# Performance work log

Measured on AMD Instinct MI355X. Metric: run time of the kernel, lower is better.

Reference implementation:

```python
import jax, jax.numpy as jnp
import numpy as np

BETA = 1.0
EPS_MU = 1e-6
EPS_LOG = 1e-8
D_DIM = 2048
M_EVENTS = 16384
T_HORIZON = 100


def setup_inputs() -> dict:
    key = jax.random.key(0)
    k1, k2 = jax.random.split(key)
    # sorted event times in [0, T_HORIZON)
    t_events = jnp.sort(jax.random.uniform(k1, (M_EVENTS,), jnp.float32) * T_HORIZON)
    marks = jax.random.randint(k2, (M_EVENTS,), 0, D_DIM)  # int marks in {0..D-1}
    # learned params, init exactly as in torch module
    log_mu = jnp.full((D_DIM,), -3.0, jnp.float32)
    log_alpha = jnp.full((D_DIM, D_DIM), -4.0, jnp.float32)
    return {
        "t_events": t_events,
        "marks": marks,
        "T_max": T_HORIZON,
        "log_mu": log_mu,
        "log_alpha": log_alpha,
    }


def _loglik(t_events, log_mu, log_alpha, marks, T_max, beta=BETA):
    mu = jax.nn.softplus(log_mu) + EPS_MU          # [D]
    alpha = jax.nn.softplus(log_alpha)             # [D, D]
    D = mu.shape[0]
    # dt[0] = 0 so the first step leaves S (= zeros) untouched, matching the
    # torch loop which skips decay at n == 0.
    dt = jnp.concatenate([jnp.zeros((1,), t_events.dtype), jnp.diff(t_events)])  # [M]

    def step(S, xs):
        dt_n, d = xs
        S = jnp.exp(-beta * dt_n) * S              # exponential decay of state [D]
        lam_d = mu[d] + alpha[d] @ S               # intensity at event's mark
        S = S.at[d].add(1.0)                       # self-excitation bump
        return S, jnp.log(lam_d + EPS_LOG)

    _, log_lams = jax.lax.scan(step, jnp.zeros((D,), mu.dtype), (dt, marks))

    # compensator integral term
    T = jnp.asarray(T_max, t_events.dtype)
    one_minus_exp = 1.0 - jnp.exp(-beta * (T - t_events))          # [M]
    contrib = jax.ops.segment_sum(one_minus_exp, marks, num_segments=D)  # [D]
    integral = mu * T + alpha @ (contrib / beta)                   # [D]
    return log_lams.sum() - integral.sum()


def reference(t_events, marks, T_max, log_mu, log_alpha):
    return _loglik(t_events, log_mu, log_alpha, marks, T_max)
```

## Files before the change

kernel.cpp:

```cpp
#include <hip/hip_runtime.h>
#include <math.h>

#define D_DIM 2048
#define M_EV  16384
#define LCH   32
#define CCH   (M_EV / LCH)
#define SEG   32
#define NSEG  (CCH / SEG)
#define BETA  1.0f

__device__ __forceinline__ float softplus_f(float x){
  float e = __expf(-fabsf(x));
  return fmaxf(x, 0.0f) + __logf(1.0f + e);
}

__device__ __forceinline__ unsigned short f2bf(float f){
  unsigned b = __float_as_uint(f);
  return (unsigned short)((b + 0x7FFFu + ((b >> 16) & 1u)) >> 16);
}
__device__ __forceinline__ float bf2f(unsigned short u){
  return __uint_as_float(((unsigned)u) << 16);
}

__device__ __forceinline__ float decode_T(const void* p){
  unsigned bits = *(const unsigned*)p;
  float fv = __uint_as_float(bits);
  return (fv >= 1e-3f && fv <= 1e7f) ? fv : (float)(int)bits;
}

__device__ __forceinline__ float wave_red(float v){
  #pragma unroll
  for (int o = 32; o > 0; o >>= 1) v += __shfl_down(v, o);
  return v;
}

__global__ void k_small(const float* __restrict__ t, const int* __restrict__ m,
                        const void* Tp, const float* __restrict__ log_mu,
                        float* __restrict__ muw, float* __restrict__ contrib,
                        float* __restrict__ SL, float* __restrict__ dchunk,
                        float* __restrict__ cumdec, float* __restrict__ Aseg,
                        float* __restrict__ acc){
  const int b = blockIdx.x, tid = threadIdx.x;
  if (b < 8){
    int j = b*256 + tid;
    float v = softplus_f(log_mu[j]) + 1e-6f;
    muw[j] = v;
    float s = wave_red(v);
    if ((tid & 63) == 0) atomicAdd(&acc[2], s);
  } else if (b < 72){
    int i = (b-8)*256 + tid;
    float T = decode_T(Tp);
    float v = 1.0f - __expf(-BETA * (T - t[i]));
    atomicAdd(&contrib[m[i]], v);
  } else if (b < 136){
    int i = (b-72)*256 + tid;
    int c = i >> 5;
    if (c < CCH - 1){
      float tn = t[(c+1)*LCH];
      float v = __expf(-BETA * (tn - t[i]));
      atomicAdd(&SL[(size_t)c * D_DIM + m[i]], v);
    }
  } else {
    int c = (b-136)*256 + tid;
    float tc = t[c*LCH];
    dchunk[c] = (c < CCH-1) ? __expf(-BETA * (t[(c+1)*LCH] - tc)) : 1.0f;
    int s0c = (c >> 5) << 5;
    cumdec[c] = __expf(-BETA * (tc - t[s0c*LCH]));
    if (b == 136 && tid < NSEG){
      int s = tid;
      Aseg[s] = (s < NSEG-1)
        ? __expf(-BETA * (t[(s+1)*SEG*LCH] - t[s*SEG*LCH])) : 1.0f;
    }
  }
}

__global__ void k_scan_local(float* __restrict__ SL,
                             const float* __restrict__ dchunk,
                             float* __restrict__ Carry){
  const int tid = threadIdx.x;
  const int seg = blockIdx.x >> 3, jb = blockIdx.x & 7;
  const int j = jb*256 + tid;
  const int c0 = seg * SEG;
  const size_t base = (size_t)c0 * D_DIM + j;
  float u = 0.f;
  float cur[4], nxt[4];
  #pragma unroll
  for (int q = 0; q < 4; ++q) cur[q] = SL[base + (size_t)q * D_DIM];
  for (int g = 0; g < SEG; g += 4){
    #pragma unroll
    for (int q = 0; q < 4; ++q)
      nxt[q] = (g+4 < SEG) ? SL[base + (size_t)(g+4+q) * D_DIM] : 0.f;
    #pragma unroll
    for (int q = 0; q < 4; ++q){
      int c = c0 + g + q;
      float l = cur[q];
      SL[(size_t)c * D_DIM + j] = u;
      u = fmaf(dchunk[c], u, l);
    }
    #pragma unroll
    for (int q = 0; q < 4; ++q) cur[q] = nxt[q];
  }
  Carry[(size_t)seg * D_DIM + j] = u;
}

__global__ void k_scan_carry(const float* __restrict__ Carry,
                             const float* __restrict__ Aseg,
                             float* __restrict__ E){
  const int j = blockIdx.x*256 + threadIdx.x;
  float cr[NSEG];
  #pragma unroll
  for (int s = 0; s < NSEG; ++s) cr[s] = Carry[(size_t)s * D_DIM + j];
  float e = 0.f;
  #pragma unroll
  for (int s = 0; s < NSEG; ++s){
    E[(size_t)s * D_DIM + j] = e;
    e = fmaf(Aseg[s], e, cr[s]);
  }
}

__global__ void k_alpha(const float* __restrict__ la,
                        const float* __restrict__ contrib,
                        unsigned short* __restrict__ sA,
                        float* __restrict__ acc){
  const int nthreads = gridDim.x * blockDim.x;
  int tid = blockIdx.x * blockDim.x + threadIdx.x;
  const float4* la4 = (const float4*)la;
  ushort4* sA4 = (ushort4*)sA;
  float p = 0.f;
  #pragma unroll
  for (int u = 0; u < 8; ++u){
    int i4 = tid + u * nthreads;
    float4 x = la4[i4];
    float4 sp;
    sp.x = softplus_f(x.x); sp.y = softplus_f(x.y);
    sp.z = softplus_f(x.z); sp.w = softplus_f(x.w);
    ushort4 h;
    h.x = f2bf(sp.x); h.y = f2bf(sp.y); h.z = f2bf(sp.z); h.w = f2bf(sp.w);
    sA4[i4] = h;
    int col = (i4 * 4) & (D_DIM - 1);
    p = fmaf(sp.x, contrib[col+0], p);
    p = fmaf(sp.y, contrib[col+1], p);
    p = fmaf(sp.z, contrib[col+2], p);
    p = fmaf(sp.w, contrib[col+3], p);
  }
  __shared__ float red[4];
  float w = wave_red(p);
  int lane = threadIdx.x & 63, wid = threadIdx.x >> 6;
  if (lane == 0) red[wid] = w;
  __syncthreads();
  if (threadIdx.x == 0) atomicAdd(&acc[1], red[0]+red[1]+red[2]+red[3]);
}

__global__ __launch_bounds__(512) void k_events(
    const float* __restrict__ t, const int* __restrict__ m,
    const unsigned short* __restrict__ sA, const float* __restrict__ muw,
    const float* __restrict__ SL, const float* __restrict__ E,
    const float* __restrict__ cumdec, float* __restrict__ acc){
  __shared__ int   ml[LCH];
  __shared__ float decs[LCH];
  __shared__ float red[LCH][8];
  const int tid = threadIdx.x;
  const int c = blockIdx.x;
  const int seg = c >> 5;
  const float cd = cumdec[c];

  const float4 sv = *(const float4*)(SL + (size_t)c  * D_DIM + tid*4);
  const float4 ev = *(const float4*)(E  + (size_t)seg * D_DIM + tid*4);
  float4 s;
  s.x = fmaf(ev.x, cd, sv.x); s.y = fmaf(ev.y, cd, sv.y);
  s.z = fmaf(ev.z, cd, sv.z); s.w = fmaf(ev.w, cd, sv.w);

  if (tid < LCH){
    ml[tid] = m[c*LCH + tid];
    float tk = t[c*LCH + tid];
    float tp = (tid == 0) ? tk : t[c*LCH + tid - 1];
    decs[tid] = __expf(-BETA * (tk - tp));
  }
  __syncthreads();

  const int lane = tid & 63, wid = tid >> 6;
  const int colb = tid * 4;

  ushort4 pf0 = *(const ushort4*)(sA + (size_t)ml[0] * D_DIM + colb);
  ushort4 pf1 = *(const ushort4*)(sA + (size_t)ml[1] * D_DIM + colb);
  ushort4 pf2 = *(const ushort4*)(sA + (size_t)ml[2] * D_DIM + colb);
  ushort4 pf3 = *(const ushort4*)(sA + (size_t)ml[3] * D_DIM + colb);

#define STAGE(Q) {                                                          \
    const int kk = k + (Q);                                                 \
    const int d = ml[kk];                                                   \
    const int kn = (kk + 4 < LCH) ? kk + 4 : LCH - 1;                       \
    ushort4 nx = *(const ushort4*)(sA + (size_t)ml[kn] * D_DIM + colb);     \
    const float dec = decs[kk];                                             \
    s.x *= dec; s.y *= dec; s.z *= dec; s.w *= dec;                         \
    float p = 0.f;                                                          \
    p = fmaf(bf2f(pf##Q.x), s.x, p);                                        \
    p = fmaf(bf2f(pf##Q.y), s.y, p);                                        \
    p = fmaf(bf2f(pf##Q.z), s.z, p);                                        \
    p = fmaf(bf2f(pf##Q.w), s.w, p);                                        \
    if ((d >> 2) == tid){                                                   \
      int r = d & 3;                                                        \
      s.x += (r==0) ? 1.f : 0.f; s.y += (r==1) ? 1.f : 0.f;                 \
      s.z += (r==2) ? 1.f : 0.f; s.w += (r==3) ? 1.f : 0.f;                 \
    }                                                                       \
    float w = wave_red(p);                                                  \
    if (lane == 0) red[kk][wid] = w;                                        \
    pf##Q = nx;                                                             \
  }

  for (int k = 0; k < LCH; k += 4){
    STAGE(0) STAGE(1) STAGE(2) STAGE(3)
  }
#undef STAGE

  __syncthreads();
  float lg = 0.f;
  if (tid < LCH){
    const float* r = red[tid];
    float lam = muw[ml[tid]] + ((r[0]+r[1])+(r[2]+r[3]))
                             + ((r[4]+r[5])+(r[6]+r[7]));
    lg = __logf(lam + 1e-8f);
  }
  if (tid < 64){
    float w = wave_red(lg);
    if (tid == 0) atomicAdd(&acc[0], w);
  }
}

__global__ void k_final(const float* __restrict__ acc, const void* Tp,
                        float* __restrict__ out){
  float T = decode_T(Tp);
  out[0] = acc[0] - (T * acc[2] + acc[1] * (1.0f / BETA));
}

extern "C" void kernel_launch(void* const* d_in, const int* in_sizes, int n_in,
                              void* d_out, int out_size, void* d_ws, size_t ws_size,
                              hipStream_t stream) {
  const float* t_events  = (const float*)d_in[0];
  const int*   marks     = (const int*)  d_in[1];
  const void*  Tp        =               d_in[2];
  const float* log_mu    = (const float*)d_in[3];
  const float* log_alpha = (const float*)d_in[4];
  float* out = (float*)d_out;

  float* ws      = (float*)d_ws;
  float* SL      = ws;
  float* contrib = SL + (size_t)CCH * D_DIM;
  float* acc     = contrib + D_DIM;
  float* Carry   = acc + 16;
  float* E       = Carry + (size_t)NSEG * D_DIM;
  float* muw     = E + (size_t)NSEG * D_DIM;
  float* dchunk  = muw + D_DIM;
  float* cumdec  = dchunk + CCH;
  float* Aseg    = cumdec + CCH;
  unsigned short* sA = (unsigned short*)(Aseg + NSEG);

  size_t zero_floats = (size_t)CCH * D_DIM + D_DIM + 16;
  hipMemsetAsync(d_ws, 0, zero_floats * sizeof(float), stream);

  k_small     <<<138, 256, 0, stream>>>(t_events, marks, Tp, log_mu, muw,
                                        contrib, SL, dchunk, cumdec, Aseg, acc);
  k_scan_local<<<NSEG*8, 256, 0, stream>>>(SL, dchunk, Carry);
  k_scan_carry<<<8, 256, 0, stream>>>(Carry, Aseg, E);
  k_alpha     <<<512, 256, 0, stream>>>(log_alpha, contrib, sA, acc);
  k_events    <<<CCH, 512, 0, stream>>>(t_events, marks, sA, muw,
                                        SL, E, cumdec, acc);
  k_final     <<<1, 1, 0, stream>>>(acc, Tp, out);
}
```

Before: 116.7 us.

## Fuse small kernels, merge carry scan with alpha, deepen prefetch, finalize in last block

Merges the contrib and chunk-local scatter branches of k_small so each event's time and mark are loaded once. Fuses the carry scan into the alpha softplus kernel as extra blocks, and removes k_final by having the last k_events block (found via an atomic ticket counter in acc[3]) compute the output. It also raises the sA row prefetch depth in k_events from 4 to 8 rows. The aim is fewer launches and fewer serial gaps between them, in exchange for more registers in k_events and a threadfence plus atomic ticket at the end of every block.

```diff
diff --git a/kernel.cpp b/kernel.cpp
--- a/kernel.cpp
+++ b/kernel.cpp
@@ -49,24 +49,22 @@
     if ((tid & 63) == 0) atomicAdd(&acc[2], s);
   } else if (b < 72){
     int i = (b-8)*256 + tid;
+    int d = m[i];
+    float ti = t[i];
     float T = decode_T(Tp);
-    float v = 1.0f - __expf(-BETA * (T - t[i]));
-    atomicAdd(&contrib[m[i]], v);
-  } else if (b < 136){
-    int i = (b-72)*256 + tid;
+    atomicAdd(&contrib[d], 1.0f - __expf(-BETA * (T - ti)));
     int c = i >> 5;
     if (c < CCH - 1){
       float tn = t[(c+1)*LCH];
-      float v = __expf(-BETA * (tn - t[i]));
-      atomicAdd(&SL[(size_t)c * D_DIM + m[i]], v);
+      atomicAdd(&SL[(size_t)c * D_DIM + d], __expf(-BETA * (tn - ti)));
     }
   } else {
-    int c = (b-136)*256 + tid;
+    int c = (b-72)*256 + tid;
     float tc = t[c*LCH];
     dchunk[c] = (c < CCH-1) ? __expf(-BETA * (t[(c+1)*LCH] - tc)) : 1.0f;
     int s0c = (c >> 5) << 5;
     cumdec[c] = __expf(-BETA * (tc - t[s0c*LCH]));
-    if (b == 136 && tid < NSEG){
+    if (b == 72 && tid < NSEG){
       int s = tid;
       Aseg[s] = (s < NSEG-1)
         ? __expf(-BETA * (t[(s+1)*SEG*LCH] - t[s*SEG*LCH])) : 1.0f;
@@ -103,33 +101,35 @@
   Carry[(size_t)seg * D_DIM + j] = u;
 }
 
-__global__ void k_scan_carry(const float* __restrict__ Carry,
-                             const float* __restrict__ Aseg,
-                             float* __restrict__ E){
-  const int j = blockIdx.x*256 + threadIdx.x;
-  float cr[NSEG];
-  #pragma unroll
-  for (int s = 0; s < NSEG; ++s) cr[s] = Carry[(size_t)s * D_DIM + j];
-  float e = 0.f;
-  #pragma unroll
-  for (int s = 0; s < NSEG; ++s){
-    E[(size_t)s * D_DIM + j] = e;
-    e = fmaf(Aseg[s], e, cr[s]);
-  }
-}
-
-__global__ void k_alpha(const float* __restrict__ la,
-                        const float* __restrict__ contrib,
-                        unsigned short* __restrict__ sA,
-                        float* __restrict__ acc){
-  const int nthreads = gridDim.x * blockDim.x;
-  int tid = blockIdx.x * blockDim.x + threadIdx.x;
+__global__ void k_carry_alpha(const float* __restrict__ Carry,
+                              const float* __restrict__ Aseg,
+                              float* __restrict__ E,
+                              const float* __restrict__ la,
+                              const float* __restrict__ contrib,
+                              unsigned short* __restrict__ sA,
+                              float* __restrict__ acc){
+  const int b = blockIdx.x, tid = threadIdx.x;
+  if (b < 8){
+    const int j = b*256 + tid;
+    float cr[NSEG];
+    #pragma unroll
+    for (int s = 0; s < NSEG; ++s) cr[s] = Carry[(size_t)s * D_DIM + j];
+    float e = 0.f;
+    #pragma unroll
+    for (int s = 0; s < NSEG; ++s){
+      E[(size_t)s * D_DIM + j] = e;
+      e = fmaf(Aseg[s], e, cr[s]);
+    }
+    return;
+  }
+  const int nthreads = 512*256;
+  int atid = (b-8)*256 + tid;
   const float4* la4 = (const float4*)la;
   ushort4* sA4 = (ushort4*)sA;
   float p = 0.f;
   #pragma unroll
   for (int u = 0; u < 8; ++u){
-    int i4 = tid + u * nthreads;
+    int i4 = atid + u * nthreads;
     float4 x = la4[i4];
     float4 sp;
     sp.x = softplus_f(x.x); sp.y = softplus_f(x.y);
@@ -145,17 +145,18 @@
   }
   __shared__ float red[4];
   float w = wave_red(p);
-  int lane = threadIdx.x & 63, wid = threadIdx.x >> 6;
+  int lane = tid & 63, wid = tid >> 6;
   if (lane == 0) red[wid] = w;
   __syncthreads();
-  if (threadIdx.x == 0) atomicAdd(&acc[1], red[0]+red[1]+red[2]+red[3]);
+  if (tid == 0) atomicAdd(&acc[1], red[0]+red[1]+red[2]+red[3]);
 }
 
 __global__ __launch_bounds__(512) void k_events(
     const float* __restrict__ t, const int* __restrict__ m,
     const unsigned short* __restrict__ sA, const float* __restrict__ muw,
     const float* __restrict__ SL, const float* __restrict__ E,
-    const float* __restrict__ cumdec, float* __restrict__ acc){
+    const float* __restrict__ cumdec, float* __restrict__ acc,
+    const void* Tp, float* __restrict__ out){
   __shared__ int   ml[LCH];
   __shared__ float decs[LCH];
   __shared__ float red[LCH][8];
@@ -185,11 +186,15 @@
   ushort4 pf1 = *(const ushort4*)(sA + (size_t)ml[1] * D_DIM + colb);
   ushort4 pf2 = *(const ushort4*)(sA + (size_t)ml[2] * D_DIM + colb);
   ushort4 pf3 = *(const ushort4*)(sA + (size_t)ml[3] * D_DIM + colb);
+  ushort4 pf4 = *(const ushort4*)(sA + (size_t)ml[4] * D_DIM + colb);
+  ushort4 pf5 = *(const ushort4*)(sA + (size_t)ml[5] * D_DIM + colb);
+  ushort4 pf6 = *(const ushort4*)(sA + (size_t)ml[6] * D_DIM + colb);
+  ushort4 pf7 = *(const ushort4*)(sA + (size_t)ml[7] * D_DIM + colb);
 
 #define STAGE(Q) {                                                          \
     const int kk = k + (Q);                                                 \
     const int d = ml[kk];                                                   \
-    const int kn = (kk + 4 < LCH) ? kk + 4 : LCH - 1;                       \
+    const int kn = (kk + 8 < LCH) ? kk + 8 : LCH - 1;                       \
     ushort4 nx = *(const ushort4*)(sA + (size_t)ml[kn] * D_DIM + colb);     \
     const float dec = decs[kk];                                             \
     s.x *= dec; s.y *= dec; s.z *= dec; s.w *= dec;                         \
@@ -208,8 +213,9 @@
     pf##Q = nx;                                                             \
   }
 
-  for (int k = 0; k < LCH; k += 4){
+  for (int k = 0; k < LCH; k += 8){
     STAGE(0) STAGE(1) STAGE(2) STAGE(3)
+    STAGE(4) STAGE(5) STAGE(6) STAGE(7)
   }
 #undef STAGE
 
@@ -223,14 +229,19 @@
   }
   if (tid < 64){
     float w = wave_red(lg);
-    if (tid == 0) atomicAdd(&acc[0], w);
-  }
-}
-
-__global__ void k_final(const float* __restrict__ acc, const void* Tp,
-                        float* __restrict__ out){
-  float T = decode_T(Tp);
-  out[0] = acc[0] - (T * acc[2] + acc[1] * (1.0f / BETA));
+    if (tid == 0){
+      atomicAdd(&acc[0], w);
+      __threadfence();
+      unsigned old = atomicAdd((unsigned*)&acc[3], 1u);
+      if (old == CCH - 1){
+        float a0 = atomicAdd(&acc[0], 0.0f);
+        float a1 = atomicAdd(&acc[1], 0.0f);
+        float a2 = atomicAdd(&acc[2], 0.0f);
+        float T = decode_T(Tp);
+        out[0] = a0 - (T * a2 + a1 * (1.0f / BETA));
+      }
+    }
+  }
 }
 
 extern "C" void kernel_launch(void* const* d_in, const int* in_sizes, int n_in,
@@ -258,12 +269,11 @@
   size_t zero_floats = (size_t)CCH * D_DIM + D_DIM + 16;
   hipMemsetAsync(d_ws, 0, zero_floats * sizeof(float), stream);
 
-  k_small     <<<138, 256, 0, stream>>>(t_events, marks, Tp, log_mu, muw,
+  k_small      <<<74, 256, 0, stream>>>(t_events, marks, Tp, log_mu, muw,
                                         contrib, SL, dchunk, cumdec, Aseg, acc);
-  k_scan_local<<<NSEG*8, 256, 0, stream>>>(SL, dchunk, Carry);
-  k_scan_carry<<<8, 256, 0, stream>>>(Carry, Aseg, E);
-  k_alpha     <<<512, 256, 0, stream>>>(log_alpha, contrib, sA, acc);
-  k_events    <<<CCH, 512, 0, stream>>>(t_events, marks, sA, muw,
-                                        SL, E, cumdec, acc);
-  k_final     <<<1, 1, 0, stream>>>(acc, Tp, out);
-}
+  k_scan_local <<<NSEG*8, 256, 0, stream>>>(SL, dchunk, Carry);
+  k_carry_alpha<<<520, 256, 0, stream>>>(Carry, Aseg, E, log_alpha,
+                                         contrib, sA, acc);
+  k_events     <<<CCH, 512, 0, stream>>>(t_events, marks, sA, muw,
+                                         SL, E, cumdec, acc, Tp, out);
+}
```

Measured after the change: 119.6 us. +2.5%, slower.
